# Kernel tuning notes

Measured on AMD Instinct MI355X. Metric: run time of the kernel, lower is better.

The kernel has to match this reference:

```python
import jax, jax.numpy as jnp
import numpy as np

NUM_HEADS = 8


def setup_inputs() -> dict:
    key = jax.random.key(0)
    k1, k2 = jax.random.split(key)
    C, B, N, D = 3, 2, 4096, 512
    x = jax.random.normal(k1, (C, B, N, D), dtype=jnp.float32)
    proj_w = jax.random.normal(k2, (D, D), dtype=jnp.float32) * (D ** -0.5)
    proj_b = jnp.zeros((D,), dtype=jnp.float32)
    return {"x": x, "proj_w": proj_w, "proj_b": proj_b}


def reference(x, proj_w, proj_b):
    C, B, N, D = x.shape
    H = NUM_HEADS
    hd = D // H
    scale = hd ** -0.5
    # [3, B, N, H, hd] -> [3, B, H, N, hd]
    xh = x.reshape(C, B, N, H, hd).transpose(0, 1, 3, 2, 4)
    q, k, v = xh[0], xh[1], xh[2]
    # attention scores [B, H, N, N]
    attn = jnp.einsum('bhqd,bhkd->bhqk', q, k) * scale
    attn = jax.nn.softmax(attn, axis=-1)
    out = jnp.einsum('bhqk,bhkd->bhqd', attn, v)  # [B, H, N, hd]
    out = out.transpose(0, 2, 1, 3).reshape(B, N, D)
    # nn.Linear: y = x @ W^T + b
    return out @ proj_w.T + proj_b
```

## Files before the change

### kernel.cpp

```cpp
#include <hip/hip_runtime.h>
#include <hip/hip_bf16.h>

typedef __attribute__((ext_vector_type(8))) short short8;
typedef __attribute__((ext_vector_type(4))) float f32x4;
typedef __attribute__((ext_vector_type(16))) float f32x16;
typedef __attribute__((ext_vector_type(4))) unsigned uint4v;

#define MFMA16(a, b, c) __builtin_amdgcn_mfma_f32_16x16x32_bf16((a), (b), (c), 0, 0, 0)
#define MFMA32(a, b, c) __builtin_amdgcn_mfma_f32_32x32x16_bf16((a), (b), (c), 0, 0, 0)

#define NB 2
#define NSEQ 4096
#define DMODEL 512
#define NH 8
#define HD 64
#define CSTRIDE (NB * NSEQ * DMODEL)

#define QSCALE 0.18033688011112042f

static __device__ __forceinline__ unsigned short f2bf(float f) {
    unsigned u = __builtin_bit_cast(unsigned, f);
    u += 0x7fffu + ((u >> 16) & 1u);
    return (unsigned short)(u >> 16);
}

static __device__ __forceinline__ short8 cvt8(float4 a, float4 b) {
    short8 r;
    r[0] = (short)f2bf(a.x); r[1] = (short)f2bf(a.y);
    r[2] = (short)f2bf(a.z); r[3] = (short)f2bf(a.w);
    r[4] = (short)f2bf(b.x); r[5] = (short)f2bf(b.y);
    r[6] = (short)f2bf(b.z); r[7] = (short)f2bf(b.w);
    return r;
}

static __device__ __forceinline__ unsigned cvt_pk_bf16(float lo, float hi) {
    unsigned r;
    asm("v_cvt_pk_bf16_f32 %0, %1, %2" : "=v"(r) : "v"(lo), "v"(hi));
    return r;
}

__global__ __launch_bounds__(256)
void qk_convert(const float* __restrict__ x, unsigned short* __restrict__ Qbf,
                unsigned short* __restrict__ Kbf) {
    int cid = blockIdx.x * 256 + threadIdx.x;
    int d8 = cid & 63;
    int n = (cid >> 6) & 4095;
    int b = (cid >> 18) & 1;
    int c = cid >> 19;
    const float* src = x + (size_t)c * CSTRIDE + ((size_t)(b * 4096 + n)) * 512 + d8 * 8;
    float4 a0 = *reinterpret_cast<const float4*>(src);
    float4 a1 = *reinterpret_cast<const float4*>(src + 4);
    float sc = c ? 1.0f : QSCALE;
    a0.x *= sc; a0.y *= sc; a0.z *= sc; a0.w *= sc;
    a1.x *= sc; a1.y *= sc; a1.z *= sc; a1.w *= sc;
    unsigned short* dst = (c ? Kbf : Qbf) +
        (((size_t)(b * 8 + (d8 >> 3)) * 4096 + n) * 64 + (d8 & 7) * 8);
    *reinterpret_cast<short8*>(dst) = cvt8(a0, a1);
}

__global__ __launch_bounds__(256)
void v_transpose(const float* __restrict__ x, unsigned short* __restrict__ Vt) {
    __shared__ __attribute__((aligned(16))) unsigned short T[64 * 66];
    unsigned* T32 = reinterpret_cast<unsigned*>(T);

    const int tid = threadIdx.x;
    const int bh = blockIdx.y;
    const int b = bh >> 3, h = bh & 7;
    const int n0 = blockIdx.x * 64;

#pragma unroll
    for (int j = 0; j < 2; ++j) {
        int cid = tid + 256 * j;
        int ni = cid >> 3;
        int d0 = (cid & 7) * 8;
        const float* src = x + (size_t)2 * CSTRIDE +
            ((size_t)(b * 4096 + n0 + ni)) * 512 + h * 64 + d0;
        float4 a0 = *reinterpret_cast<const float4*>(src);
        float4 a1 = *reinterpret_cast<const float4*>(src + 4);
        short8 v = cvt8(a0, a1);
#pragma unroll
        for (int k = 0; k < 4; ++k) {
            unsigned pk = (unsigned)(unsigned short)v[2 * k] |
                          ((unsigned)(unsigned short)v[2 * k + 1] << 16);
            T32[ni * 33 + (d0 >> 1) + k] = pk;
        }
    }
    __syncthreads();

#pragma unroll
    for (int j = 0; j < 2; ++j) {
        int cid = tid + 256 * j;
        int di = cid >> 3;
        int k0 = (cid & 7) * 8;
        short8 o;
#pragma unroll
        for (int k = 0; k < 8; ++k) o[k] = (short)T[(k0 + k) * 66 + di];
        unsigned short* dst = Vt + ((size_t)(bh * 64 + di)) * 4096 + n0 + k0;
        *reinterpret_cast<short8*>(dst) = o;
    }
}

__global__ __launch_bounds__(256)
void w_convert(const float* __restrict__ W, unsigned short* __restrict__ Wbf) {
    int cid = blockIdx.x * 256 + threadIdx.x;
    int d8 = cid & 63;
    int row = cid >> 6;
    const float* src = W + (size_t)row * 512 + d8 * 8;
    float4 a0 = *reinterpret_cast<const float4*>(src);
    float4 a1 = *reinterpret_cast<const float4*>(src + 4);
    *reinterpret_cast<short8*>(Wbf + (size_t)row * 512 + d8 * 8) = cvt8(a0, a1);
}

__global__ __launch_bounds__(256, 2)
void attn_kernel(const unsigned short* __restrict__ Qbf,
                 const unsigned short* __restrict__ Kbf,
                 const unsigned short* __restrict__ Vt,
                 unsigned short* __restrict__ Obf) {
    __shared__ __attribute__((aligned(16))) unsigned char SMEM[16384];

    const int tid = threadIdx.x;
    const int lane = tid & 63;
    const int wv = tid >> 6;
    const int hi = lane >> 5;
    const int l5 = lane & 31;

    const int bh = blockIdx.y;
    const int b = bh >> 3, h = bh & 7;
    const int qbase = blockIdx.x * 256 + wv * 64;

    const unsigned short* Qh = Qbf + (size_t)bh * NSEQ * HD;
    const unsigned short* Kh = Kbf + (size_t)bh * NSEQ * HD;
    const unsigned short* Vh = Vt + (size_t)bh * HD * NSEQ;

    short8 qf[2][4];
#pragma unroll
    for (int u = 0; u < 2; ++u)
#pragma unroll
        for (int c = 0; c < 4; ++c)
            qf[u][c] = *reinterpret_cast<const short8*>(
                Qh + (size_t)(qbase + u * 32 + l5) * HD + c * 16 + hi * 8);

    f32x16 oacc[2][2];
#pragma unroll
    for (int u = 0; u < 2; ++u)
#pragma unroll
        for (int db = 0; db < 2; ++db)
#pragma unroll
            for (int r = 0; r < 16; ++r) oacc[u][db][r] = 0.f;
    float l_run[2] = {0.f, 0.f};

    const int row0 = tid >> 3;
    const int row1 = row0 + 32;
    const int e0 = (tid & 7) * 8;

    const int o0 = (row0 * 128 + e0 * 2) ^ ((row0 & 7) << 4);
    const int o1 = (row1 * 128 + e0 * 2) ^ ((row1 & 7) << 4);
    const int swz = (l5 & 7) << 4;

    char* K_lds = (char*)SMEM;
    char* V_lds = (char*)SMEM + 8192;

    short8 kreg[2], vreg[2];
    kreg[0] = *reinterpret_cast<const short8*>(Kh + (size_t)row0 * HD + e0);
    kreg[1] = *reinterpret_cast<const short8*>(Kh + (size_t)row1 * HD + e0);
    vreg[0] = *reinterpret_cast<const short8*>(Vh + (size_t)row0 * NSEQ + e0);
    vreg[1] = *reinterpret_cast<const short8*>(Vh + (size_t)row1 * NSEQ + e0);

    for (int kt = 0; kt < 64; ++kt) {
        __syncthreads();
        *reinterpret_cast<short8*>(K_lds + o0) = kreg[0];
        *reinterpret_cast<short8*>(K_lds + o1) = kreg[1];
        *reinterpret_cast<short8*>(V_lds + o0) = vreg[0];
        *reinterpret_cast<short8*>(V_lds + o1) = vreg[1];
        {
            int nt = (kt + 1) & 63;
            kreg[0] = *reinterpret_cast<const short8*>(Kh + (size_t)(nt * 64 + row0) * HD + e0);
            kreg[1] = *reinterpret_cast<const short8*>(Kh + (size_t)(nt * 64 + row1) * HD + e0);
            vreg[0] = *reinterpret_cast<const short8*>(Vh + (size_t)row0 * NSEQ + nt * 64 + e0);
            vreg[1] = *reinterpret_cast<const short8*>(Vh + (size_t)row1 * NSEQ + nt * 64 + e0);
        }
        __syncthreads();

        f32x16 st[2][2];
        __builtin_amdgcn_s_setprio(1);
#pragma unroll
        for (int kb = 0; kb < 2; ++kb) {
            f32x16 aA, aB;
#pragma unroll
            for (int r = 0; r < 16; ++r) { aA[r] = 0.f; aB[r] = 0.f; }
#pragma unroll
            for (int c = 0; c < 4; ++c) {
                int key = kb * 32 + l5;
                short8 kf = *reinterpret_cast<const short8*>(
                    K_lds + ((key * 128 + c * 32 + hi * 16) ^ swz));
                aA = MFMA32(kf, qf[0][c], aA);
                aB = MFMA32(kf, qf[1][c], aB);
            }
            st[0][kb] = aA;
            st[1][kb] = aB;
        }
        __builtin_amdgcn_s_setprio(0);

#pragma unroll
        for (int u = 0; u < 2; ++u) {
#pragma unroll
            for (int kb = 0; kb < 2; ++kb)
#pragma unroll
                for (int r = 0; r < 16; ++r)
                    st[u][kb][r] = __builtin_amdgcn_exp2f(st[u][kb][r]);
            float s = 0.f;
#pragma unroll
            for (int r = 0; r < 16; ++r) s += st[u][0][r] + st[u][1][r];
            s += __shfl_xor(s, 32);
            l_run[u] += s;
        }

        short8 PA[2][4];
#pragma unroll
        for (int u = 0; u < 2; ++u)
#pragma unroll
            for (int kb = 0; kb < 2; ++kb)
#pragma unroll
                for (int ks = 0; ks < 2; ++ks) {
                    unsigned c0 = cvt_pk_bf16(st[u][kb][8 * ks + 0], st[u][kb][8 * ks + 1]);
                    unsigned c1 = cvt_pk_bf16(st[u][kb][8 * ks + 2], st[u][kb][8 * ks + 3]);
                    unsigned c2 = cvt_pk_bf16(st[u][kb][8 * ks + 4], st[u][kb][8 * ks + 5]);
                    unsigned c3 = cvt_pk_bf16(st[u][kb][8 * ks + 6], st[u][kb][8 * ks + 7]);
                    unsigned d0 = (unsigned)__shfl_xor((int)c0, 32);
                    unsigned d1 = (unsigned)__shfl_xor((int)c1, 32);
                    unsigned d2 = (unsigned)__shfl_xor((int)c2, 32);
                    unsigned d3 = (unsigned)__shfl_xor((int)c3, 32);
                    uint4v w;
                    w[0] = hi ? d2 : c0;
                    w[1] = hi ? d3 : c1;
                    w[2] = hi ? c2 : d0;
                    w[3] = hi ? c3 : d1;
                    PA[u][kb * 2 + ks] = __builtin_bit_cast(short8, w);
                }

        __builtin_amdgcn_s_setprio(1);
#pragma unroll
        for (int ch = 0; ch < 4; ++ch) {
#pragma unroll
            for (int db = 0; db < 2; ++db) {
                int d = db * 32 + l5;
                short8 vf = *reinterpret_cast<const short8*>(
                    V_lds + ((d * 128 + ch * 32 + hi * 16) ^ swz));
                oacc[0][db] = MFMA32(PA[0][ch], vf, oacc[0][db]);
                oacc[1][db] = MFMA32(PA[1][ch], vf, oacc[1][db]);
            }
        }
        __builtin_amdgcn_s_setprio(0);
    }

#pragma unroll
    for (int u = 0; u < 2; ++u) {
#pragma unroll
        for (int r = 0; r < 16; ++r) {
            int crow = (r & 3) + 8 * (r >> 2) + 4 * hi;
            float inv = 1.0f / __shfl(l_run[u], crow);
            int qrow = qbase + u * 32 + crow;
            size_t obase = (size_t)(b * NSEQ + qrow) * DMODEL + h * HD;
            Obf[obase + l5] = f2bf(oacc[u][0][r] * inv);
            Obf[obase + 32 + l5] = f2bf(oacc[u][1][r] * inv);
        }
    }
}

__global__ __launch_bounds__(256, 4)
void proj_kernel(const unsigned short* __restrict__ Obf, const unsigned short* __restrict__ Wbf,
                 const float* __restrict__ bias, float* __restrict__ out) {
    __shared__ __attribute__((aligned(16))) unsigned short W_lds[64 * 64];

    const int tid = threadIdx.x;
    const int lane = tid & 63;
    const int wv = tid >> 6;
    const int g = lane >> 4;
    const int l4 = lane & 15;

    const int bm = blockIdx.x;
    const int bn = blockIdx.y;

    f32x4 acc[4];
#pragma unroll
    for (int jt = 0; jt < 4; ++jt) acc[jt] = (f32x4){0.f, 0.f, 0.f, 0.f};

    for (int kc = 0; kc < DMODEL / 64; ++kc) {
#pragma unroll
        for (int j = 0; j < 2; ++j) {
            int cid = tid + 256 * j;
            int row = cid >> 3;
            int ee = (cid & 7) * 8;
            short8 wv8 = *reinterpret_cast<const short8*>(
                Wbf + (size_t)(bn * 64 + row) * DMODEL + kc * 64 + ee);
            int off = (row * 128 + ee * 2) ^ ((row & 7) << 4);
            *reinterpret_cast<short8*>((char*)W_lds + off) = wv8;
        }
        __syncthreads();

#pragma unroll
        for (int sub = 0; sub < 2; ++sub) {
            const unsigned short* ap =
                Obf + (size_t)(bm * 64 + wv * 16 + l4) * DMODEL + kc * 64 + sub * 32 + g * 8;
            short8 a = *reinterpret_cast<const short8*>(ap);
#pragma unroll
            for (int jt = 0; jt < 4; ++jt) {
                int jj = jt * 16 + l4;
                int off = (jj * 128 + (sub * 32 + g * 8) * 2) ^ ((jj & 7) << 4);
                short8 wb = *reinterpret_cast<const short8*>((const char*)W_lds + off);
                acc[jt] = MFMA16(a, wb, acc[jt]);
            }
        }
        __syncthreads();
    }

#pragma unroll
    for (int jt = 0; jt < 4; ++jt) {
        int jg = bn * 64 + jt * 16 + l4;
        float bj = bias[jg];
#pragma unroll
        for (int r = 0; r < 4; ++r) {
            int ig = bm * 64 + wv * 16 + g * 4 + r;
            out[(size_t)ig * DMODEL + jg] = acc[jt][r] + bj;
        }
    }
}

extern "C" void kernel_launch(void* const* d_in, const int* in_sizes, int n_in,
                              void* d_out, int out_size, void* d_ws, size_t ws_size,
                              hipStream_t stream) {
    const float* x = (const float*)d_in[0];
    const float* W = (const float*)d_in[1];
    const float* bias = (const float*)d_in[2];
    float* out = (float*)d_out;

    char* ws = (char*)d_ws;
    unsigned short* Obf = (unsigned short*)(ws);
    unsigned short* Qbf = (unsigned short*)(ws + (8u << 20));
    unsigned short* Kbf = (unsigned short*)(ws + (16u << 20));
    unsigned short* Vt = (unsigned short*)(ws + (24u << 20));
    unsigned short* Wbf = (unsigned short*)(ws + (32u << 20));

    qk_convert<<<4096, 256, 0, stream>>>(x, Qbf, Kbf);
    v_transpose<<<dim3(NSEQ / 64, NB * NH), 256, 0, stream>>>(x, Vt);
    w_convert<<<128, 256, 0, stream>>>(W, Wbf);

    dim3 gA(NSEQ / 256, NB * NH);
    attn_kernel<<<gA, 256, 0, stream>>>(Qbf, Kbf, Vt, Obf);

    dim3 gP(NB * NSEQ / 64, DMODEL / 64);
    proj_kernel<<<gP, 256, 0, stream>>>(Obf, Wbf, bias, out);
}
```

Measured before the change: 137.8 us.

## Split the key range across wave pairs in attention and merge partial outputs

Each attention block now covers 128 queries instead of 256. Its two wave pairs each process half of the key sequence, staging K and V into their own shared-memory buffers. The partial accumulators and row sums are combined through shared memory before normalisation and the bf16 store. This doubles the grid so more blocks are spread across the CUs, at the cost of more K/V reads overall, double the shared memory per block, and an extra cross-wave reduction at the end.

```diff
diff --git a/kernel.cpp b/kernel.cpp
--- a/kernel.cpp
+++ b/kernel.cpp
@@ -111,27 +111,34 @@
     *reinterpret_cast<short8*>(Wbf + (size_t)row * 512 + d8 * 8) = cvt8(a0, a1);
 }
 
+#define SMEM_BYTES (32768 + 512)
+
 __global__ __launch_bounds__(256, 2)
 void attn_kernel(const unsigned short* __restrict__ Qbf,
                  const unsigned short* __restrict__ Kbf,
                  const unsigned short* __restrict__ Vt,
                  unsigned short* __restrict__ Obf) {
-    __shared__ __attribute__((aligned(16))) unsigned char SMEM[16384];
+    __shared__ __attribute__((aligned(16))) unsigned char SMEM[SMEM_BYTES];
 
     const int tid = threadIdx.x;
     const int lane = tid & 63;
     const int wv = tid >> 6;
     const int hi = lane >> 5;
     const int l5 = lane & 31;
+    const int half = wv >> 1;
+    const int qs = wv & 1;
 
     const int bh = blockIdx.y;
     const int b = bh >> 3, h = bh & 7;
-    const int qbase = blockIdx.x * 256 + wv * 64;
+    const int qbase = blockIdx.x * 128 + qs * 64;
 
     const unsigned short* Qh = Qbf + (size_t)bh * NSEQ * HD;
     const unsigned short* Kh = Kbf + (size_t)bh * NSEQ * HD;
     const unsigned short* Vh = Vt + (size_t)bh * HD * NSEQ;
 
+    char* K_lds = (char*)SMEM + half * 16384;
+    char* V_lds = K_lds + 8192;
+
     short8 qf[2][4];
 #pragma unroll
     for (int u = 0; u < 2; ++u)
@@ -149,35 +156,41 @@
             for (int r = 0; r < 16; ++r) oacc[u][db][r] = 0.f;
     float l_run[2] = {0.f, 0.f};
 
-    const int row0 = tid >> 3;
-    const int row1 = row0 + 32;
-    const int e0 = (tid & 7) * 8;
-
-    const int o0 = (row0 * 128 + e0 * 2) ^ ((row0 & 7) << 4);
-    const int o1 = (row1 * 128 + e0 * 2) ^ ((row1 & 7) << 4);
+    const int gt = tid & 127;
+    const int kt0 = half * 32;
+    int srow[4], se0[4], soff[4];
+#pragma unroll
+    for (int c = 0; c < 4; ++c) {
+        int chunk = gt + 128 * c;
+        srow[c] = chunk >> 3;
+        se0[c] = (chunk & 7) * 8;
+        soff[c] = (srow[c] * 128 + se0[c] * 2) ^ ((srow[c] & 7) << 4);
+    }
     const int swz = (l5 & 7) << 4;
 
-    char* K_lds = (char*)SMEM;
-    char* V_lds = (char*)SMEM + 8192;
-
-    short8 kreg[2], vreg[2];
-    kreg[0] = *reinterpret_cast<const short8*>(Kh + (size_t)row0 * HD + e0);
-    kreg[1] = *reinterpret_cast<const short8*>(Kh + (size_t)row1 * HD + e0);
-    vreg[0] = *reinterpret_cast<const short8*>(Vh + (size_t)row0 * NSEQ + e0);
-    vreg[1] = *reinterpret_cast<const short8*>(Vh + (size_t)row1 * NSEQ + e0);
-
-    for (int kt = 0; kt < 64; ++kt) {
+    short8 kreg[4], vreg[4];
+#pragma unroll
+    for (int c = 0; c < 4; ++c) {
+        kreg[c] = *reinterpret_cast<const short8*>(Kh + (size_t)(kt0 * 64 + srow[c]) * HD + se0[c]);
+        vreg[c] = *reinterpret_cast<const short8*>(Vh + (size_t)srow[c] * NSEQ + kt0 * 64 + se0[c]);
+    }
+
+    for (int step = 0; step < 32; ++step) {
         __syncthreads();
-        *reinterpret_cast<short8*>(K_lds + o0) = kreg[0];
-        *reinterpret_cast<short8*>(K_lds + o1) = kreg[1];
-        *reinterpret_cast<short8*>(V_lds + o0) = vreg[0];
-        *reinterpret_cast<short8*>(V_lds + o1) = vreg[1];
+#pragma unroll
+        for (int c = 0; c < 4; ++c) {
+            *reinterpret_cast<short8*>(K_lds + soff[c]) = kreg[c];
+            *reinterpret_cast<short8*>(V_lds + soff[c]) = vreg[c];
+        }
         {
-            int nt = (kt + 1) & 63;
-            kreg[0] = *reinterpret_cast<const short8*>(Kh + (size_t)(nt * 64 + row0) * HD + e0);
-            kreg[1] = *reinterpret_cast<const short8*>(Kh + (size_t)(nt * 64 + row1) * HD + e0);
-            vreg[0] = *reinterpret_cast<const short8*>(Vh + (size_t)row0 * NSEQ + nt * 64 + e0);
-            vreg[1] = *reinterpret_cast<const short8*>(Vh + (size_t)row1 * NSEQ + nt * 64 + e0);
+            int nt = kt0 + ((step + 1) & 31);
+#pragma unroll
+            for (int c = 0; c < 4; ++c) {
+                kreg[c] = *reinterpret_cast<const short8*>(
+                    Kh + (size_t)(nt * 64 + srow[c]) * HD + se0[c]);
+                vreg[c] = *reinterpret_cast<const short8*>(
+                    Vh + (size_t)srow[c] * NSEQ + nt * 64 + se0[c]);
+            }
         }
         __syncthreads();
 
@@ -253,16 +266,40 @@
         __builtin_amdgcn_s_setprio(0);
     }
 
-#pragma unroll
-    for (int u = 0; u < 2; ++u) {
-#pragma unroll
-        for (int r = 0; r < 16; ++r) {
-            int crow = (r & 3) + 8 * (r >> 2) + 4 * hi;
-            float inv = 1.0f / __shfl(l_run[u], crow);
-            int qrow = qbase + u * 32 + crow;
-            size_t obase = (size_t)(b * NSEQ + qrow) * DMODEL + h * HD;
-            Obf[obase + l5] = f2bf(oacc[u][0][r] * inv);
-            Obf[obase + 32 + l5] = f2bf(oacc[u][1][r] * inv);
+    float* Xo = (float*)SMEM;
+    float* Xl = (float*)(SMEM + 32768);
+
+    __syncthreads();
+    if (half == 1) {
+#pragma unroll
+        for (int u = 0; u < 2; ++u) {
+#pragma unroll
+            for (int r = 0; r < 16; ++r) {
+                int crow = (r & 3) + 8 * (r >> 2) + 4 * hi;
+                int qloc = qs * 64 + u * 32 + crow;
+                Xo[qloc * 64 + l5] = oacc[u][0][r];
+                Xo[qloc * 64 + 32 + l5] = oacc[u][1][r];
+            }
+            if (hi == 0) Xl[qs * 64 + u * 32 + l5] = l_run[u];
+        }
+    }
+    __syncthreads();
+    if (half == 0) {
+#pragma unroll
+        for (int u = 0; u < 2; ++u) {
+#pragma unroll
+            for (int r = 0; r < 16; ++r) {
+                int crow = (r & 3) + 8 * (r >> 2) + 4 * hi;
+                int qloc = qs * 64 + u * 32 + crow;
+                float l1 = Xl[qloc];
+                float inv = 1.0f / (__shfl(l_run[u], crow) + l1);
+                float v0 = oacc[u][0][r] + Xo[qloc * 64 + l5];
+                float v1 = oacc[u][1][r] + Xo[qloc * 64 + 32 + l5];
+                int qrow = qbase + u * 32 + crow;
+                size_t obase = (size_t)(b * NSEQ + qrow) * DMODEL + h * HD;
+                Obf[obase + l5] = f2bf(v0 * inv);
+                Obf[obase + 32 + l5] = f2bf(v1 * inv);
+            }
         }
     }
 }
@@ -345,7 +382,7 @@
     v_transpose<<<dim3(NSEQ / 64, NB * NH), 256, 0, stream>>>(x, Vt);
     w_convert<<<128, 256, 0, stream>>>(W, Wbf);
 
-    dim3 gA(NSEQ / 256, NB * NH);
+    dim3 gA(NSEQ / 128, NB * NH);
     attn_kernel<<<gA, 256, 0, stream>>>(Qbf, Kbf, Vt, Obf);
 
     dim3 gP(NB * NSEQ / 64, DMODEL / 64);
```

After: 138.7 us. No clear change (+0.6%).
